# Kernel tuning notes

Hardware: AMD Instinct MI355X
Metric: run time of the kernel (lower is better)

## Reference

```python
import jax, jax.numpy as jnp
import numpy as np

DIM = 1024
NUM_HEADS = 16
HEAD_DIM = DIM // NUM_HEADS
BATCH = 2
SEQ = 2048
ROPE_BASE = 10000.0


def _rope_cos_sin(seq_len, head_dim, dtype=jnp.float32):
    inv_freq = 1.0 / (ROPE_BASE ** (jnp.arange(0, head_dim, 2, dtype=jnp.float32) / head_dim))
    t = jnp.arange(seq_len, dtype=jnp.float32)
    freqs = jnp.outer(t, inv_freq)              # (S, D/2)
    emb = jnp.concatenate([freqs, freqs], axis=-1)  # (S, D)
    return jnp.cos(emb).astype(dtype), jnp.sin(emb).astype(dtype)


def _rotate_half(x):
    x1, x2 = jnp.split(x, 2, axis=-1)
    return jnp.concatenate([-x2, x1], axis=-1)


def _apply_rope(x, cos, sin):
    # x: (B, S, H, D); cos/sin: (S, D) -> broadcast (1, S, 1, D)
    cos = cos[None, :, None, :]
    sin = sin[None, :, None, :]
    return x * cos + _rotate_half(x) * sin


def setup_inputs() -> dict:
    key = jax.random.key(0)
    ks = jax.random.split(key, 5)
    x = jax.random.normal(ks[0], (BATCH, SEQ, DIM), dtype=jnp.float32)
    scale = DIM ** -0.5
    wq = jax.random.normal(ks[1], (DIM, DIM), dtype=jnp.float32) * scale
    wk = jax.random.normal(ks[2], (DIM, DIM), dtype=jnp.float32) * scale
    wv = jax.random.normal(ks[3], (DIM, DIM), dtype=jnp.float32) * scale
    wo = jax.random.normal(ks[4], (DIM, DIM), dtype=jnp.float32) * scale
    return {"x": x, "wq": wq, "wk": wk, "wv": wv, "wo": wo}


def reference(x, wq, wk, wv, wo):
    B, S, _ = x.shape
    scale = HEAD_DIM ** -0.5
    # nn.Linear(x) = x @ W.T; weights stored (out, in)
    q = (x @ wq.T).reshape(B, S, NUM_HEADS, HEAD_DIM)
    k = (x @ wk.T).reshape(B, S, NUM_HEADS, HEAD_DIM)
    v = (x @ wv.T).reshape(B, S, NUM_HEADS, HEAD_DIM)
    cos, sin = _rope_cos_sin(S, HEAD_DIM, x.dtype)
    q = _apply_rope(q, cos, sin)
    k = _apply_rope(k, cos, sin)
    # (B, H, S, S) scores, full softmax attention (no mask, dropout=0)
    scores = jnp.einsum('bqhd,bkhd->bhqk', q, k) * scale
    attn = jax.nn.softmax(scores, axis=-1)
    out = jnp.einsum('bhqk,bkhd->bqhd', attn, v).reshape(B, S, DIM)
    return out @ wo.T
```

## Files before the change

kernel.cpp:

```cpp
#include <hip/hip_runtime.h>
#include <hip/hip_bf16.h>
#include <stdint.h>


#define AS1(p) ((const __attribute__((address_space(1))) void*)(p))
#define AS3(p) ((__attribute__((address_space(3))) void*)(p))

typedef __attribute__((ext_vector_type(8)))  __bf16 bf16x8;
typedef __attribute__((ext_vector_type(4)))  float  f32x4;
typedef __attribute__((ext_vector_type(16))) float  f32x16;

__device__ __forceinline__ ushort f2b(float f) {
  union { float f; uint32_t u; } v; v.f = f;
  uint32_t u = v.u;
  u += 0x7fffu + ((u >> 16) & 1);
  return (ushort)(u >> 16);
}
__device__ __forceinline__ float b2f(ushort s) {
  union { uint32_t u; float f; } v; v.u = ((uint32_t)s) << 16;
  return v.f;
}
__device__ __forceinline__ uint32_t pkbf16(float lo, float hi) {
  uint32_t w;
  asm("v_cvt_pk_bf16_f32 %0, %1, %2" : "=v"(w) : "v"(lo), "v"(hi));
  return w;
}
__device__ __forceinline__ float fast_exp2(float x) {
#if __has_builtin(__builtin_amdgcn_exp2f)
  return __builtin_amdgcn_exp2f(x);
#else
  float r;
  asm("v_exp_f32 %0, %1\n\ts_nop 1" : "=v"(r) : "v"(x));
  return r;
#endif
}

__global__ __launch_bounds__(256) void cvt_all_k(
    const float* __restrict__ x,  const float* __restrict__ wq,
    const float* __restrict__ wk, const float* __restrict__ wv,
    const float* __restrict__ wo, ushort* __restrict__ dst,
    float2* __restrict__ tab) {
  for (int it = 0; it < 4; it++) {
    int i = (it * 2048 + blockIdx.x) * 256 + threadIdx.x;
    const float* src;
    if      (i < 1048576) src = x  + (size_t)i * 4;
    else if (i < 1310720) src = wq + (size_t)(i - 1048576) * 4;
    else if (i < 1572864) src = wk + (size_t)(i - 1310720) * 4;
    else if (i < 1835008) src = wv + (size_t)(i - 1572864) * 4;
    else                  src = wo + (size_t)(i - 1835008) * 4;
    float4 v = *(const float4*)src;
    ushort4 o;
    o.x = f2b(v.x); o.y = f2b(v.y); o.z = f2b(v.z); o.w = f2b(v.w);
    ((ushort4*)dst)[i] = o;

    if (i < 65536) {
      int s = i >> 5, dp = i & 31;
      float inv = exp2f((float)dp * (-13.2877123795494f / 32.0f));
      float ang = (float)s * inv;
      float sn, cs;
      sincosf(ang, &sn, &cs);
      tab[i] = make_float2(cs, sn);
    }
  }
}

__device__ __forceinline__ void gemm_mainloop(
    const ushort* __restrict__ A, const ushort* __restrict__ W,
    int row0, int col0, ushort* lds, f32x4 acc[4][4]) {
  const int K = 1024;
  int tid = threadIdx.x;
  int lane = tid & 63, wid = tid >> 6;
  int wr = wid >> 1, wc = wid & 1;
  int lr = lane >> 4, lc = lane & 15;
  ushort* lA = lds;
  ushort* lB = lds + 8192;

  auto stage = [&](int buf, int k0) {
#pragma unroll
    for (int i = 0; i < 2; i++) {
      int idx = tid + i * 256;
      const ushort* ga = A + (size_t)(row0 + (idx >> 2)) * K + k0 + (idx & 3) * 8;
      __builtin_amdgcn_global_load_lds(AS1(ga),
          AS3(lA + buf * 4096 + (i * 256 + wid * 64) * 8), 16, 0, 0);
      const ushort* gb = W + (size_t)(col0 + (idx >> 2)) * K + k0 + (idx & 3) * 8;
      __builtin_amdgcn_global_load_lds(AS1(gb),
          AS3(lB + buf * 4096 + (i * 256 + wid * 64) * 8), 16, 0, 0);
    }
  };

  stage(0, 0);
  __syncthreads();
  int cur = 0;
  for (int k0 = 0; k0 < K; k0 += 32) {
    if (k0 + 32 < K) stage(cur ^ 1, k0 + 32);
    const ushort* a  = lA + cur * 4096;
    const ushort* bm = lB + cur * 4096;
    bf16x8 af[4], bfr[4];
#pragma unroll
    for (int m = 0; m < 4; m++)
      af[m] = *(const bf16x8*)(a + (wr * 64 + m * 16 + lc) * 32 + lr * 8);
#pragma unroll
    for (int n = 0; n < 4; n++)
      bfr[n] = *(const bf16x8*)(bm + (wc * 64 + n * 16 + lc) * 32 + lr * 8);
#pragma unroll
    for (int m = 0; m < 4; m++)
#pragma unroll
      for (int n = 0; n < 4; n++)
        acc[m][n] = __builtin_amdgcn_mfma_f32_16x16x32_bf16(af[m], bfr[n], acc[m][n], 0, 0, 0);
    __syncthreads();
    cur ^= 1;
  }
}

__global__ __launch_bounds__(256) void gemm_qkv_k(
    const ushort* __restrict__ xb,
    const ushort* __restrict__ wqb, const ushort* __restrict__ wkb,
    const ushort* __restrict__ wvb,
    const float2* __restrict__ tab,
    ushort* __restrict__ Qb, ushort* __restrict__ Kb, ushort* __restrict__ Vtb) {
  __shared__ ushort lds[16384];
  int z = blockIdx.z;
  const ushort* w = (z == 0) ? wqb : (z == 1) ? wkb : wvb;
  int row0 = blockIdx.x * 128, col0 = blockIdx.y * 128;
  f32x4 acc[4][4] = {};
  gemm_mainloop(xb, w, row0, col0, lds, acc);

  int tid = threadIdx.x, lane = tid & 63, wid = tid >> 6;
  int wr = wid >> 1, wc = wid & 1, lr = lane >> 4, lc = lane & 15;

  if (z < 2) {
    ushort* dst = (z == 0) ? Qb : Kb;
    const float qs = (z == 0) ? 0.125f * 1.44269504088896f : 1.0f;
#pragma unroll
    for (int m = 0; m < 4; m++)
#pragma unroll
      for (int n = 0; n < 2; n++)
#pragma unroll
        for (int j = 0; j < 4; j++) {
          int i = row0 + wr * 64 + m * 16 + lr * 4 + j;
          int c = col0 + wc * 64 + n * 16 + lc;
          int b = i >> 11, s = i & 2047, h = c >> 6, dp = c & 31;
          float2 cs = tab[s * 32 + dp];
          float q1 = acc[m][n][j], q2 = acc[m][n + 2][j];
          float r1 = (q1 * cs.x - q2 * cs.y) * qs;
          float r2 = (q2 * cs.x + q1 * cs.y) * qs;
          size_t base = (size_t)(b * 16 + h) * 131072 + (size_t)s * 64;
          dst[base + dp]      = f2b(r1);
          dst[base + dp + 32] = f2b(r2);
        }
  } else {
#pragma unroll
    for (int m = 0; m < 4; m++)
#pragma unroll
      for (int n = 0; n < 4; n++) {
        int c = wc * 64 + n * 16 + lc;
        int sb = wr * 64 + m * 16 + lr * 4;
        uint32_t w0 = pkbf16(acc[m][n][0], acc[m][n][1]);
        uint32_t w1 = pkbf16(acc[m][n][2], acc[m][n][3]);
        int soff = sb ^ ((c & 7) << 3);
        uint2 val; val.x = w0; val.y = w1;
        *(uint2*)(lds + c * 128 + soff) = val;
      }
    __syncthreads();
    int b = row0 >> 11, srow = row0 & 2047;
#pragma unroll
    for (int i = 0; i < 8; i++) {
      int idx = i * 256 + tid;
      int cl = idx >> 4, sc = idx & 15;
      int soff = (sc * 8) ^ ((cl & 7) << 3);
      bf16x8 v = *(const bf16x8*)(lds + cl * 128 + soff);
      int cg = col0 + cl, h = cg >> 6, d = cg & 63;
      *(bf16x8*)(Vtb + (size_t)(b * 16 + h) * 131072 + (size_t)d * 2048 + srow + sc * 8) = v;
    }
  }
}

__global__ __launch_bounds__(256) void gemm_out_k(
    const ushort* __restrict__ Ab, const ushort* __restrict__ wob,
    float* __restrict__ out) {
  __shared__ ushort lds[12288];
  const int K = 1024;
  int tid = threadIdx.x, lane = tid & 63, wid = tid >> 6;
  int lr = lane >> 4, lc = lane & 15;
  int row0 = blockIdx.x * 128, col0 = blockIdx.y * 64;
  ushort* lA = lds;
  ushort* lB = lds + 8192;

  auto stage = [&](int buf, int k0) {
#pragma unroll
    for (int i = 0; i < 2; i++) {
      int idx = tid + i * 256;
      const ushort* ga = Ab + (size_t)(row0 + (idx >> 2)) * K + k0 + (idx & 3) * 8;
      __builtin_amdgcn_global_load_lds(AS1(ga),
          AS3(lA + buf * 4096 + (i * 256 + wid * 64) * 8), 16, 0, 0);
    }
    const ushort* gb = wob + (size_t)(col0 + (tid >> 2)) * K + k0 + (tid & 3) * 8;
    __builtin_amdgcn_global_load_lds(AS1(gb),
        AS3(lB + buf * 2048 + wid * 512), 16, 0, 0);
  };

  f32x4 acc[2][4] = {};
  stage(0, 0);
  __syncthreads();
  int cur = 0;
  for (int k0 = 0; k0 < K; k0 += 32) {
    if (k0 + 32 < K) stage(cur ^ 1, k0 + 32);
    const ushort* a  = lA + cur * 4096;
    const ushort* bm = lB + cur * 2048;
    bf16x8 af[2], bfr[4];
#pragma unroll
    for (int m = 0; m < 2; m++)
      af[m] = *(const bf16x8*)(a + (wid * 32 + m * 16 + lc) * 32 + lr * 8);
#pragma unroll
    for (int n = 0; n < 4; n++)
      bfr[n] = *(const bf16x8*)(bm + (n * 16 + lc) * 32 + lr * 8);
#pragma unroll
    for (int m = 0; m < 2; m++)
#pragma unroll
      for (int n = 0; n < 4; n++)
        acc[m][n] = __builtin_amdgcn_mfma_f32_16x16x32_bf16(af[m], bfr[n], acc[m][n], 0, 0, 0);
    __syncthreads();
    cur ^= 1;
  }

  int base_r = row0 + wid * 32;
#pragma unroll
  for (int m = 0; m < 2; m++)
#pragma unroll
    for (int n = 0; n < 4; n++)
#pragma unroll
      for (int j = 0; j < 4; j++) {
        int i = base_r + m * 16 + lr * 4 + j;
        int c = col0 + n * 16 + lc;
        out[(size_t)i * 1024 + c] = acc[m][n][j];
      }
}

__global__ __launch_bounds__(512, 4) void attn_k(
    const ushort* __restrict__ Qb, const ushort* __restrict__ Kb,
    const ushort* __restrict__ Vtb, ushort* __restrict__ Ob) {
  __shared__ char ldsb[65536];
  int tid = threadIdx.x, lane = tid & 63, wid = tid >> 6;
  int lc5 = lane & 31, hi = lane >> 5;
  int qsub = wid & 3, grp = wid >> 2;

  int bid = blockIdx.x;
  int qt = (bid >> 3) & 15;
  int bh = (bid & 7) + ((bid >> 7) << 3);
  int q0 = qt * 128 + qsub * 32;
  const ushort* Qp = Qb  + (size_t)bh * 131072 + (size_t)q0 * 64;
  const ushort* Kp = Kb  + (size_t)bh * 131072;
  const ushort* Vp = Vtb + (size_t)bh * 131072;

  bf16x8 qf[4];
#pragma unroll
  for (int ks = 0; ks < 4; ks++)
    qf[ks] = *(const bf16x8*)(Qp + lc5 * 64 + ks * 16 + hi * 8);

  f32x16 o0, o1;
#pragma unroll
  for (int i = 0; i < 16; i++) { o0[i] = 0.f; o1[i] = 0.f; }
  float lsum = 0.f;

  int swz[4];
#pragma unroll
  for (int ks = 0; ks < 4; ks++)
    swz[ks] = (((2 * ks + hi) ^ (lc5 & 7)) << 4);
  const int rbase = lc5 * 128;

  auto stage = [&](int buf, int kvp) {
    int r = tid >> 3, cp = tid & 7;
    int ubase = wid * 1024;
#pragma unroll
    for (int t = 0; t < 2; t++) {
      char* tb = ldsb + buf * 32768 + t * 16384;
      const ushort* gk = Kp + (size_t)(kvp + 64 * t + r) * 64 + ((cp ^ (r & 7)) << 3);
      __builtin_amdgcn_global_load_lds(AS1(gk), AS3(tb + ubase), 16, 0, 0);
      const ushort* gv = Vp + (size_t)r * 2048 + kvp + 64 * t + ((cp ^ (r & 7)) << 3);
      __builtin_amdgcn_global_load_lds(AS1(gv), AS3(tb + 8192 + ubase), 16, 0, 0);
    }
  };

  auto smpack = [&](f32x16& s, bf16x8* aout) {
#pragma unroll
    for (int i = 0; i < 16; i++) s[i] = fast_exp2(s[i]);
    float acc = 0.f;
#pragma unroll
    for (int i = 0; i < 16; i++) acc += s[i];
    lsum += acc;
#pragma unroll
    for (int h2 = 0; h2 < 2; h2++) {
      int rb = 8 * h2;
      uint32_t wa1 = pkbf16(s[rb],     s[rb + 1]);
      uint32_t wb1 = pkbf16(s[rb + 4], s[rb + 5]);
      asm("v_permlane32_swap_b32 %0, %1" : "+v"(wa1), "+v"(wb1));
      uint32_t wa2 = pkbf16(s[rb + 2], s[rb + 3]);
      uint32_t wb2 = pkbf16(s[rb + 6], s[rb + 7]);
      asm("v_permlane32_swap_b32 %0, %1" : "+v"(wa2), "+v"(wb2));
      union { uint32_t u[4]; bf16x8 v; } tmp;
      tmp.u[0] = wa1; tmp.u[1] = wa2; tmp.u[2] = wb1; tmp.u[3] = wb2;
      aout[h2] = tmp.v;
    }
  };

  stage(0, 0);
  stage(1, 128);
  int cur = 0;

  for (int kvp = 0; kvp < 2048; kvp += 128) {
    if (kvp + 128 < 2048) asm volatile("s_waitcnt vmcnt(4)" ::: "memory");
    else                  asm volatile("s_waitcnt vmcnt(0)" ::: "memory");
    asm volatile("s_barrier" ::: "memory");

    const char* kbuf = ldsb + cur * 32768 + grp * 16384;
    const char* vbuf = kbuf + 8192;

    f32x16 s0 = {}, s1 = {};
    __builtin_amdgcn_s_setprio(1);
#pragma unroll
    for (int ks = 0; ks < 4; ks++) {
      bf16x8 ka0 = *(const bf16x8*)(kbuf + rbase + swz[ks]);
      s0 = __builtin_amdgcn_mfma_f32_32x32x16_bf16(ka0, qf[ks], s0, 0, 0, 0);
    }
#pragma unroll
    for (int ks = 0; ks < 4; ks++) {
      bf16x8 ka1 = *(const bf16x8*)(kbuf + 4096 + rbase + swz[ks]);
      s1 = __builtin_amdgcn_mfma_f32_32x32x16_bf16(ka1, qf[ks], s1, 0, 0, 0);
    }
    __builtin_amdgcn_s_setprio(0);

    bf16x8 a01[2], a23[2];
    smpack(s0, a01);

    __builtin_amdgcn_s_setprio(1);
#pragma unroll
    for (int ks = 0; ks < 2; ks++) {
      bf16x8 vb0 = *(const bf16x8*)(vbuf + rbase + swz[ks]);
      bf16x8 vb1 = *(const bf16x8*)(vbuf + 4096 + rbase + swz[ks]);
      o0 = __builtin_amdgcn_mfma_f32_32x32x16_bf16(a01[ks], vb0, o0, 0, 0, 0);
      o1 = __builtin_amdgcn_mfma_f32_32x32x16_bf16(a01[ks], vb1, o1, 0, 0, 0);
    }
    __builtin_amdgcn_s_setprio(0);

    smpack(s1, a23);

    __builtin_amdgcn_s_setprio(1);
#pragma unroll
    for (int ks = 2; ks < 4; ks++) {
      bf16x8 vb0 = *(const bf16x8*)(vbuf + rbase + swz[ks]);
      bf16x8 vb1 = *(const bf16x8*)(vbuf + 4096 + rbase + swz[ks]);
      o0 = __builtin_amdgcn_mfma_f32_32x32x16_bf16(a23[ks - 2], vb0, o0, 0, 0, 0);
      o1 = __builtin_amdgcn_mfma_f32_32x32x16_bf16(a23[ks - 2], vb1, o1, 0, 0, 0);
    }
    __builtin_amdgcn_s_setprio(0);

    asm volatile("s_barrier" ::: "memory");
    if (kvp + 256 < 2048) stage(cur, kvp + 256);
    cur ^= 1;
  }

  float* cb = (float*)ldsb;
  float* p = cb + (size_t)(qsub * 64 + lane) * 33;
  if (grp == 1) {
#pragma unroll
    for (int i = 0; i < 16; i++) { p[i] = o0[i]; p[16 + i] = o1[i]; }
    p[32] = lsum;
  }
  __syncthreads();
  if (grp == 0) {
#pragma unroll
    for (int i = 0; i < 16; i++) { o0[i] += p[i]; o1[i] += p[16 + i]; }
    lsum += p[32];

    lsum += __shfl_xor(lsum, 32);
    float invq = 1.0f / lsum;
    float invr[16];
#pragma unroll
    for (int r = 0; r < 16; r++)
      invr[r] = __shfl(invq, (r & 3) + 8 * (r >> 2) + 4 * hi);

    int b = bh >> 4, h = bh & 15;
    ushort* Op = Ob + (size_t)(b * 2048 + q0) * 1024 + h * 64 + lc5;
#pragma unroll
    for (int r = 0; r < 16; r++) {
      int rrow = (r & 3) + 8 * (r >> 2) + 4 * hi;
      Op[(size_t)rrow * 1024]      = f2b(o0[r] * invr[r]);
      Op[(size_t)rrow * 1024 + 32] = f2b(o1[r] * invr[r]);
    }
  }
}

extern "C" void kernel_launch(void* const* d_in, const int* in_sizes, int n_in,
                              void* d_out, int out_size, void* d_ws, size_t ws_size,
                              hipStream_t stream) {
  const float* x  = (const float*)d_in[0];
  const float* wq = (const float*)d_in[1];
  const float* wk = (const float*)d_in[2];
  const float* wv = (const float*)d_in[3];
  const float* wo = (const float*)d_in[4];
  float* out = (float*)d_out;
  char* ws = (char*)d_ws;
  const size_t MiB = 1024 * 1024;
  ushort* xb  = (ushort*)(ws + 0);
  ushort* wqb = (ushort*)(ws + 8 * MiB);
  ushort* wkb = (ushort*)(ws + 10 * MiB);
  ushort* wvb = (ushort*)(ws + 12 * MiB);
  ushort* wob = (ushort*)(ws + 14 * MiB);
  ushort* Qb  = (ushort*)(ws + 16 * MiB);
  ushort* Kb  = (ushort*)(ws + 24 * MiB);
  ushort* Vtb = (ushort*)(ws + 32 * MiB);
  ushort* Ob  = (ushort*)(ws + 40 * MiB);
  float2* tab = (float2*)Ob;

  cvt_all_k<<<2048, 256, 0, stream>>>(x, wq, wk, wv, wo, xb, tab);
  dim3 gqkv(32, 8, 3);
  gemm_qkv_k<<<gqkv, 256, 0, stream>>>(xb, wqb, wkb, wvb, tab, Qb, Kb, Vtb);
  attn_k<<<512, 512, 0, stream>>>(Qb, Kb, Vtb, Ob);
  dim3 gout(32, 16);
  gemm_out_k<<<gout, 256, 0, stream>>>(Ob, wob, out);
}
```

Before: 102.0 us.

## Fuse x fp32-to-bf16 conversion into QKV GEMM A-tile loading

The separate conversion pass over the activation x is removed. The QKV GEMM now stages fp32 x tiles straight into LDS with a swizzled layout and packs them to bf16 in registers before the MFMA. This drops a full write and read of the bf16 copy of x and shrinks the conversion kernel to the weights only. In exchange, each of the 24 column/QKV blocks re-reads fp32 x, which doubles A-tile global traffic and LDS footprint per block and adds conversion ALU work in the inner loop.

```diff
diff --git a/kernel.cpp b/kernel.cpp
--- a/kernel.cpp
+++ b/kernel.cpp
@@ -35,19 +35,17 @@
 #endif
 }
 
-__global__ __launch_bounds__(256) void cvt_all_k(
-    const float* __restrict__ x,  const float* __restrict__ wq,
-    const float* __restrict__ wk, const float* __restrict__ wv,
-    const float* __restrict__ wo, ushort* __restrict__ dst,
-    float2* __restrict__ tab) {
-  for (int it = 0; it < 4; it++) {
+__global__ __launch_bounds__(256) void cvt_w_k(
+    const float* __restrict__ wq, const float* __restrict__ wk,
+    const float* __restrict__ wv, const float* __restrict__ wo,
+    ushort* __restrict__ dst, float2* __restrict__ tab) {
+  for (int it = 0; it < 2; it++) {
     int i = (it * 2048 + blockIdx.x) * 256 + threadIdx.x;
     const float* src;
-    if      (i < 1048576) src = x  + (size_t)i * 4;
-    else if (i < 1310720) src = wq + (size_t)(i - 1048576) * 4;
-    else if (i < 1572864) src = wk + (size_t)(i - 1310720) * 4;
-    else if (i < 1835008) src = wv + (size_t)(i - 1572864) * 4;
-    else                  src = wo + (size_t)(i - 1835008) * 4;
+    if      (i < 262144) src = wq + (size_t)i * 4;
+    else if (i < 524288) src = wk + (size_t)(i - 262144) * 4;
+    else if (i < 786432) src = wv + (size_t)(i - 524288) * 4;
+    else                 src = wo + (size_t)(i - 786432) * 4;
     float4 v = *(const float4*)src;
     ushort4 o;
     o.x = f2b(v.x); o.y = f2b(v.y); o.z = f2b(v.z); o.w = f2b(v.w);
@@ -113,20 +111,68 @@
 }
 
 __global__ __launch_bounds__(256) void gemm_qkv_k(
-    const ushort* __restrict__ xb,
+    const float* __restrict__ x,
     const ushort* __restrict__ wqb, const ushort* __restrict__ wkb,
     const ushort* __restrict__ wvb,
     const float2* __restrict__ tab,
     ushort* __restrict__ Qb, ushort* __restrict__ Kb, ushort* __restrict__ Vtb) {
-  __shared__ ushort lds[16384];
+  __shared__ char ldsq[49152];
+  const int K = 1024;
   int z = blockIdx.z;
   const ushort* w = (z == 0) ? wqb : (z == 1) ? wkb : wvb;
   int row0 = blockIdx.x * 128, col0 = blockIdx.y * 128;
-  f32x4 acc[4][4] = {};
-  gemm_mainloop(xb, w, row0, col0, lds, acc);
-
   int tid = threadIdx.x, lane = tid & 63, wid = tid >> 6;
   int wr = wid >> 1, wc = wid & 1, lr = lane >> 4, lc = lane & 15;
+  ushort* lB = (ushort*)(ldsq + 32768);
+
+  auto stage = [&](int buf, int k0) {
+#pragma unroll
+    for (int i = 0; i < 4; i++) {
+      int c = i * 256 + tid;
+      int r = c >> 3, cp = c & 7;
+      const float* ga = x + (size_t)(row0 + r) * K + k0 + ((cp ^ (r & 7)) << 2);
+      __builtin_amdgcn_global_load_lds(AS1(ga),
+          AS3(ldsq + buf * 16384 + (i * 256 + wid * 64) * 16), 16, 0, 0);
+    }
+#pragma unroll
+    for (int i = 0; i < 2; i++) {
+      int idx = tid + i * 256;
+      const ushort* gb = w + (size_t)(col0 + (idx >> 2)) * K + k0 + (idx & 3) * 8;
+      __builtin_amdgcn_global_load_lds(AS1(gb),
+          AS3(lB + buf * 4096 + (i * 256 + wid * 64) * 8), 16, 0, 0);
+    }
+  };
+
+  f32x4 acc[4][4] = {};
+  stage(0, 0);
+  __syncthreads();
+  int cur = 0;
+  for (int k0 = 0; k0 < K; k0 += 32) {
+    if (k0 + 32 < K) stage(cur ^ 1, k0 + 32);
+    const char* a = ldsq + cur * 16384;
+    const ushort* bm = lB + cur * 4096;
+    bf16x8 af[4], bfr[4];
+#pragma unroll
+    for (int m = 0; m < 4; m++) {
+      int r = wr * 64 + m * 16 + lc;
+      float4 lo = *(const float4*)(a + r * 128 + (((2 * lr)     ^ (lc & 7)) << 4));
+      float4 hi = *(const float4*)(a + r * 128 + (((2 * lr + 1) ^ (lc & 7)) << 4));
+      union { uint32_t u[4]; bf16x8 v; } t;
+      t.u[0] = pkbf16(lo.x, lo.y); t.u[1] = pkbf16(lo.z, lo.w);
+      t.u[2] = pkbf16(hi.x, hi.y); t.u[3] = pkbf16(hi.z, hi.w);
+      af[m] = t.v;
+    }
+#pragma unroll
+    for (int n = 0; n < 4; n++)
+      bfr[n] = *(const bf16x8*)(bm + (wc * 64 + n * 16 + lc) * 32 + lr * 8);
+#pragma unroll
+    for (int m = 0; m < 4; m++)
+#pragma unroll
+      for (int n = 0; n < 4; n++)
+        acc[m][n] = __builtin_amdgcn_mfma_f32_16x16x32_bf16(af[m], bfr[n], acc[m][n], 0, 0, 0);
+    __syncthreads();
+    cur ^= 1;
+  }
 
   if (z < 2) {
     ushort* dst = (z == 0) ? Qb : Kb;
@@ -149,6 +195,7 @@
           dst[base + dp + 32] = f2b(r2);
         }
   } else {
+    ushort* vls = (ushort*)ldsq;
 #pragma unroll
     for (int m = 0; m < 4; m++)
 #pragma unroll
@@ -159,7 +206,7 @@
         uint32_t w1 = pkbf16(acc[m][n][2], acc[m][n][3]);
         int soff = sb ^ ((c & 7) << 3);
         uint2 val; val.x = w0; val.y = w1;
-        *(uint2*)(lds + c * 128 + soff) = val;
+        *(uint2*)(vls + c * 128 + soff) = val;
       }
     __syncthreads();
     int b = row0 >> 11, srow = row0 & 2047;
@@ -168,7 +215,7 @@
       int idx = i * 256 + tid;
       int cl = idx >> 4, sc = idx & 15;
       int soff = (sc * 8) ^ ((cl & 7) << 3);
-      bf16x8 v = *(const bf16x8*)(lds + cl * 128 + soff);
+      bf16x8 v = *(const bf16x8*)(vls + cl * 128 + soff);
       int cg = col0 + cl, h = cg >> 6, d = cg & 63;
       *(bf16x8*)(Vtb + (size_t)(b * 16 + h) * 131072 + (size_t)d * 2048 + srow + sc * 8) = v;
     }
@@ -401,20 +448,19 @@
   float* out = (float*)d_out;
   char* ws = (char*)d_ws;
   const size_t MiB = 1024 * 1024;
-  ushort* xb  = (ushort*)(ws + 0);
-  ushort* wqb = (ushort*)(ws + 8 * MiB);
-  ushort* wkb = (ushort*)(ws + 10 * MiB);
-  ushort* wvb = (ushort*)(ws + 12 * MiB);
-  ushort* wob = (ushort*)(ws + 14 * MiB);
-  ushort* Qb  = (ushort*)(ws + 16 * MiB);
-  ushort* Kb  = (ushort*)(ws + 24 * MiB);
-  ushort* Vtb = (ushort*)(ws + 32 * MiB);
-  ushort* Ob  = (ushort*)(ws + 40 * MiB);
+  ushort* wqb = (ushort*)(ws + 0);
+  ushort* wkb = (ushort*)(ws + 2 * MiB);
+  ushort* wvb = (ushort*)(ws + 4 * MiB);
+  ushort* wob = (ushort*)(ws + 6 * MiB);
+  ushort* Qb  = (ushort*)(ws + 8 * MiB);
+  ushort* Kb  = (ushort*)(ws + 16 * MiB);
+  ushort* Vtb = (ushort*)(ws + 24 * MiB);
+  ushort* Ob  = (ushort*)(ws + 32 * MiB);
   float2* tab = (float2*)Ob;
 
-  cvt_all_k<<<2048, 256, 0, stream>>>(x, wq, wk, wv, wo, xb, tab);
+  cvt_w_k<<<2048, 256, 0, stream>>>(wq, wk, wv, wo, wqb, tab);
   dim3 gqkv(32, 8, 3);
-  gemm_qkv_k<<<gqkv, 256, 0, stream>>>(xb, wqb, wkb, wvb, tab, Qb, Kb, Vtb);
+  gemm_qkv_k<<<gqkv, 256, 0, stream>>>(x, wqb, wkb, wvb, tab, Qb, Kb, Vtb);
   attn_k<<<512, 512, 0, stream>>>(Qb, Kb, Vtb, Ob);
   dim3 gout(32, 16);
   gemm_out_k<<<gout, 256, 0, stream>>>(Ob, wob, out);
```

New measurement: 125.3 us. +22.8%, slower.
